# Kernel tuning notes

Measured on AMD Instinct MI355X. Metric: run time of the kernel, lower is better.

Reference implementation:

```python
import jax, jax.numpy as jnp
import numpy as np

N = 50000   # nodes
E = 800000  # edges
D = 128     # input feature dim
HID = 64    # hidden dim
NEG_SLOPE = 0.2


def setup_inputs() -> dict:
    key = jax.random.key(0)
    ks = jax.random.split(key, 12)
    s = 0.1
    x = jax.random.normal(ks[0], (N, D), jnp.float32)
    edge_index = jax.random.randint(ks[1], (2, E), 0, N, dtype=jnp.int64)
    # layer 1: GATConv(128 -> 64, heads=2, concat=False)
    W1 = jax.random.normal(ks[2], (D, 2 * HID), jnp.float32) * s
    a_src1 = jax.random.normal(ks[3], (2, HID), jnp.float32) * s
    a_dst1 = jax.random.normal(ks[4], (2, HID), jnp.float32) * s
    b1 = jnp.zeros((HID,), jnp.float32)
    # layer 2: GATConv(64 -> 64, heads=1, concat=False)
    W2 = jax.random.normal(ks[5], (HID, HID), jnp.float32) * s
    a_src2 = jax.random.normal(ks[6], (1, HID), jnp.float32) * s
    a_dst2 = jax.random.normal(ks[7], (1, HID), jnp.float32) * s
    b2 = jnp.zeros((HID,), jnp.float32)
    # classifier Linear(64 -> 2)
    Wc = jax.random.normal(ks[8], (HID, 2), jnp.float32) * s
    bc = jnp.zeros((2,), jnp.float32)
    return {"x": x, "edge_index": edge_index, "W1": W1, "a_src1": a_src1,
            "a_dst1": a_dst1, "b1": b1, "W2": W2, "a_src2": a_src2,
            "a_dst2": a_dst2, "b2": b2, "Wc": Wc, "bc": bc}


def _gat_layer(x, src, dst, W, a_s, a_d, b, n):
    """PyG GATConv (concat=False -> mean over heads), eval mode."""
    H, C = a_s.shape
    h = (x @ W).reshape(n, H, C)                      # [N,H,C]
    alpha_s = jnp.sum(h * a_s, axis=-1)               # [N,H]
    alpha_d = jnp.sum(h * a_d, axis=-1)               # [N,H]
    e = jax.nn.leaky_relu(alpha_s[src] + alpha_d[dst], NEG_SLOPE)  # [E,H]
    # segment softmax over incoming edges of each target node
    m = jax.ops.segment_max(e, dst, num_segments=n)   # [N,H]
    e = jnp.exp(e - m[dst])
    denom = jax.ops.segment_sum(e, dst, num_segments=n)
    alpha = e / (denom[dst] + 1e-16)                  # [E,H]
    msg = h[src] * alpha[:, :, None]                  # [E,H,C]
    out = jax.ops.segment_sum(msg, dst, num_segments=n)  # [N,H,C]
    return out.mean(axis=1) + b                       # [N,C]


def reference(x, edge_index, W1, a_src1, a_dst1, b1, W2, a_src2, a_dst2, b2, Wc, bc):
    n = x.shape[0]
    loops = jnp.arange(n, dtype=edge_index.dtype)     # PyG add_self_loops=True
    src = jnp.concatenate([edge_index[0], loops])
    dst = jnp.concatenate([edge_index[1], loops])
    h = jax.nn.elu(_gat_layer(x, src, dst, W1, a_src1, a_dst1, b1, n))
    h = jax.nn.elu(_gat_layer(h, src, dst, W2, a_src2, a_dst2, b2, n))
    logits = h @ Wc + bc
    return jax.nn.log_softmax(logits, axis=1)
```

## Files before the change

### kernel.cpp

```cpp
#include <hip/hip_runtime.h>
#include <math.h>

#define NN 50000
#define NE 800000
#define NT (NE + NN)
#define NBUCK 196
#define BE 4096
#define NBLK_B ((NT + BE - 1) / BE)
#define CAP 6144
#define NBLK_G ((NN + 63) / 64)

typedef short bf16x8 __attribute__((ext_vector_type(8)));
typedef float f32x4 __attribute__((ext_vector_type(4)));
union U16x8 { uint4 u; bf16x8 s; };

__device__ __forceinline__ unsigned pk_bf16x2(float x, float y) {
  unsigned ux = __float_as_uint(x); ux = ux + 0x7FFFu + ((ux >> 16) & 1u);
  unsigned uy = __float_as_uint(y); uy = uy + 0x7FFFu + ((uy >> 16) & 1u);
  return (ux >> 16) | (uy & 0xFFFF0000u);
}
__device__ __forceinline__ unsigned short bf16_1(float x) {
  unsigned u = __float_as_uint(x); u = u + 0x7FFFu + ((u >> 16) & 1u);
  return (unsigned short)(u >> 16);
}
__device__ __forceinline__ float blo(unsigned v) { return __uint_as_float(v << 16); }
__device__ __forceinline__ float bhi(unsigned v) { return __uint_as_float(v & 0xFFFF0000u); }

__global__ __launch_bounds__(256) void k_prep(const float* __restrict__ W1, const float* __restrict__ W2,
                                              unsigned short* __restrict__ w1f,
                                              unsigned short* __restrict__ w2f,
                                              int* __restrict__ bcur) {
  int i = blockIdx.x * 256 + threadIdx.x;
  if (i < NBUCK) bcur[i] = i * CAP;
  if (i < 128 * 128) {
    int k = i >> 7, col = i & 127;
    int ct = col >> 4, kt = k >> 5, lane = (((k >> 3) & 3) << 4) | (col & 15), j = k & 7;
    w1f[(((ct << 2) | kt) * 64 + lane) * 8 + j] = bf16_1(W1[i]);
  } else if (i < 128 * 128 + 64 * 64) {
    int e = i - 128 * 128;
    int k = e >> 6, col = e & 63;
    int ct = col >> 4, kt = k >> 5, lane = (((k >> 3) & 3) << 4) | (col & 15), j = k & 7;
    w2f[(((ct << 1) | kt) * 64 + lane) * 8 + j] = bf16_1(W2[e]);
  }
}

__global__ __launch_bounds__(256) void k_gb(
    const int* __restrict__ src, const int* __restrict__ dst,
    int* __restrict__ bcur, unsigned* __restrict__ staging,
    const float* __restrict__ x, const unsigned short* __restrict__ w1f,
    const float* __restrict__ asw_g, const float* __restrict__ adw_g,
    unsigned short* __restrict__ h1b, float* __restrict__ as1, float* __restrict__ ad1) {
  __shared__ int hist[NBUCK];
  __shared__ int base[NBUCK];
  if (blockIdx.x < NBLK_B) {
    const int t = threadIdx.x;
    const int e0 = blockIdx.x * BE;
    if (t < NBUCK) hist[t] = 0;
    __syncthreads();
    for (int j = t; j < BE; j += 256) {
      int i = e0 + j;
      if (i >= NT) break;
      int d = (i < NE) ? dst[i] : (i - NE);
      atomicAdd(&hist[d >> 8], 1);
    }
    __syncthreads();
    if (t < NBUCK) {
      int c = hist[t];
      base[t] = c ? atomicAdd(&bcur[t], c) : 0;
      hist[t] = 0;
    }
    __syncthreads();
    for (int j = t; j < BE; j += 256) {
      int i = e0 + j;
      if (i >= NT) break;
      int s, d;
      if (i < NE) { s = src[i]; d = dst[i]; } else { s = d = i - NE; }
      int b = d >> 8;
      int off = atomicAdd(&hist[b], 1);
      staging[base[b] + off] = ((unsigned)d << 16) | (unsigned)s;
    }
    return;
  }
  const int bid = blockIdx.x - NBLK_B;
  const int t = threadIdx.x;
  const int wid = t >> 6, l = t & 63;
  const int lr = l & 15, lg = l >> 4;
  const int arow = bid * 64 + wid * 16 + lr;
  const bool aok = arow < NN;

  float asw_t[8], adw_t[8];
#pragma unroll
  for (int ct = 0; ct < 8; ++ct) {
    asw_t[ct] = asw_g[ct * 16 + lr];
    adw_t[ct] = adw_g[ct * 16 + lr];
  }

  f32x4 acc[8];
#pragma unroll
  for (int ct = 0; ct < 8; ++ct) acc[ct] = (f32x4){0.f, 0.f, 0.f, 0.f};

#pragma unroll
  for (int kt = 0; kt < 4; ++kt) {
    U16x8 a;
    if (aok) {
      const float* xp = &x[(long long)arow * 128 + kt * 32 + lg * 8];
      float4 f0 = *(const float4*)xp;
      float4 f1 = *(const float4*)(xp + 4);
      a.u.x = pk_bf16x2(f0.x, f0.y); a.u.y = pk_bf16x2(f0.z, f0.w);
      a.u.z = pk_bf16x2(f1.x, f1.y); a.u.w = pk_bf16x2(f1.z, f1.w);
    } else {
      a.u = make_uint4(0, 0, 0, 0);
    }
#pragma unroll
    for (int ct = 0; ct < 8; ++ct) {
      U16x8 b;
      b.u = *(const uint4*)&w1f[(((ct << 2) | kt) * 64 + l) * 8];
      acc[ct] = __builtin_amdgcn_mfma_f32_16x16x32_bf16(a.s, b.s, acc[ct], 0, 0, 0);
    }
  }

  const int gr0 = bid * 64 + wid * 16 + lg * 4;
#pragma unroll
  for (int reg = 0; reg < 4; ++reg) {
    int grow = gr0 + reg;
    bool ok = grow < NN;
    float s0 = 0.f, s1 = 0.f, d0 = 0.f, d1 = 0.f;
#pragma unroll
    for (int ct = 0; ct < 8; ++ct) {
      float v = acc[ct][reg];
      if (ok) h1b[(long long)grow * 128 + ct * 16 + lr] = bf16_1(v);
      if (ct < 4) { s0 += v * asw_t[ct]; d0 += v * adw_t[ct]; }
      else        { s1 += v * asw_t[ct]; d1 += v * adw_t[ct]; }
    }
#pragma unroll
    for (int off = 1; off < 16; off <<= 1) {
      s0 += __shfl_xor(s0, off); d0 += __shfl_xor(d0, off);
      s1 += __shfl_xor(s1, off); d1 += __shfl_xor(d1, off);
    }
    if (ok && lr == 0) {
      as1[grow * 2] = s0; as1[grow * 2 + 1] = s1;
      ad1[grow * 2] = d0; ad1[grow * 2 + 1] = d1;
    }
  }
}

__global__ __launch_bounds__(256) void k_bscan(const int* __restrict__ bcur, int* __restrict__ bbase) {
  __shared__ int wsum[4];
  const int t = threadIdx.x;
  const int l = t & 63, w = t >> 6;
  int v = (t < NBUCK) ? bcur[t] - t * CAP : 0;
  int sc = v;
#pragma unroll
  for (int off = 1; off < 64; off <<= 1) {
    int u = __shfl_up(sc, off);
    if (l >= off) sc += u;
  }
  if (l == 63) wsum[w] = sc;
  __syncthreads();
  int wo = 0;
  for (int i = 0; i < w; ++i) wo += wsum[i];
  int incl = sc + wo;
  if (t < NBUCK) bbase[t] = incl - v;
  if (t == 255) bbase[NBUCK] = incl;
}

__global__ __launch_bounds__(256) void k_scatter2(const unsigned* __restrict__ staging,
                                                  const int* __restrict__ bcur,
                                                  const int* __restrict__ bbase,
                                                  int* __restrict__ rowptr,
                                                  unsigned short* __restrict__ csr16) {
  __shared__ int lcnt[256];
  __shared__ int wsum[4];
  const int b = blockIdx.x;
  const int t = threadIdx.x;
  const int nlo = b << 8;
  lcnt[t] = 0;
  __syncthreads();
  const int s0 = b * CAP;
  const int cnt = bcur[b] - s0;
  for (int k = t; k < cnt; k += 256)
    atomicAdd(&lcnt[(int)(staging[s0 + k] >> 16) - nlo], 1);
  __syncthreads();
  int v = lcnt[t];
  int sc = v;
  const int l = t & 63, w = t >> 6;
#pragma unroll
  for (int off = 1; off < 64; off <<= 1) {
    int u = __shfl_up(sc, off);
    if (l >= off) sc += u;
  }
  if (l == 63) wsum[w] = sc;
  __syncthreads();
  int wo = 0;
  for (int i = 0; i < w; ++i) wo += wsum[i];
  const int base = bbase[b] + sc + wo - v;
  if (nlo + t < NN) rowptr[nlo + t] = base;
  if (b == NBUCK - 1 && t == 0) rowptr[NN] = bbase[NBUCK];
  __syncthreads();
  lcnt[t] = base;
  __syncthreads();
  for (int k = t; k < cnt; k += 256) {
    unsigned e = staging[s0 + k];
    int d = (int)(e >> 16) - nlo;
    int pos = atomicAdd(&lcnt[d], 1);
    csr16[pos] = (unsigned short)(e & 0xFFFFu);
  }
}

__global__ __launch_bounds__(256) void k_gat1(
    const int* __restrict__ rowptr, const unsigned short* __restrict__ csr16,
    const unsigned* __restrict__ h1u, const float2* __restrict__ as1,
    const float2* __restrict__ ad1, const float* __restrict__ b1,
    unsigned* __restrict__ out1b) {
  __shared__ float2 sw[4][2][64];
  const int t = threadIdx.x;
  const int wv = t >> 6;
  const int n = blockIdx.x * 4 + wv;
  if (n >= NN) return;
  const int p = t & 63;
  const int h = p >> 5;
  const int beg = rowptr[n], end = rowptr[n + 1];
  const int deg = end - beg;
  const float2 adn = ad1[n];

  float acc0 = 0.f, acc1 = 0.f;
  float inv;

  if (deg <= 64) {
    int s = 0; float e0 = -1e30f, e1 = -1e30f;
    if (p < deg) {
      s = csr16[beg + p];
      float2 a = as1[s];
      e0 = a.x + adn.x; e0 = fmaxf(e0, 0.2f * e0);
      e1 = a.y + adn.y; e1 = fmaxf(e1, 0.2f * e1);
    }
    float m0 = e0, m1 = e1;
#pragma unroll
    for (int off = 1; off < 64; off <<= 1) {
      m0 = fmaxf(m0, __shfl_xor(m0, off));
      m1 = fmaxf(m1, __shfl_xor(m1, off));
    }
    float w0 = (p < deg) ? __expf(e0 - m0) : 0.f;
    float w1 = (p < deg) ? __expf(e1 - m1) : 0.f;
    float d0 = w0, d1 = w1;
#pragma unroll
    for (int off = 1; off < 64; off <<= 1) {
      d0 += __shfl_xor(d0, off);
      d1 += __shfl_xor(d1, off);
    }
    sw[wv][0][p] = make_float2(__int_as_float(s), w0);
    sw[wv][1][p] = make_float2(__int_as_float(s), w1);
    __builtin_amdgcn_wave_barrier();
    inv = 1.f / ((h ? d1 : d0) + 1e-16f);

    int j = 0;
    for (; j + 8 <= deg; j += 8) {
      float2 a[8]; unsigned v[8];
#pragma unroll
      for (int u = 0; u < 8; ++u) a[u] = sw[wv][h][j + u];
#pragma unroll
      for (int u = 0; u < 8; ++u) v[u] = h1u[(__float_as_int(a[u].x) << 6) + p];
#pragma unroll
      for (int u = 0; u < 8; ++u) {
        acc0 += a[u].y * blo(v[u]);
        acc1 += a[u].y * bhi(v[u]);
      }
    }
    if (j + 4 <= deg) {
      float2 a[4]; unsigned v[4];
#pragma unroll
      for (int u = 0; u < 4; ++u) a[u] = sw[wv][h][j + u];
#pragma unroll
      for (int u = 0; u < 4; ++u) v[u] = h1u[(__float_as_int(a[u].x) << 6) + p];
#pragma unroll
      for (int u = 0; u < 4; ++u) {
        acc0 += a[u].y * blo(v[u]);
        acc1 += a[u].y * bhi(v[u]);
      }
      j += 4;
    }
    for (; j < deg; ++j) {
      float2 a = sw[wv][h][j];
      unsigned v = h1u[(__float_as_int(a.x) << 6) + p];
      acc0 += a.y * blo(v); acc1 += a.y * bhi(v);
    }
  } else {
    float m0 = -1e30f, d0 = 0.f, m1 = -1e30f, d1 = 0.f;
    for (int k = beg + p; k < end; k += 64) {
      float2 a = as1[csr16[k]];
      float e0 = a.x + adn.x; e0 = fmaxf(e0, 0.2f * e0);
      float e1 = a.y + adn.y; e1 = fmaxf(e1, 0.2f * e1);
      if (e0 > m0) { d0 *= __expf(m0 - e0); m0 = e0; }
      d0 += __expf(e0 - m0);
      if (e1 > m1) { d1 *= __expf(m1 - e1); m1 = e1; }
      d1 += __expf(e1 - m1);
    }
#pragma unroll
    for (int off = 1; off < 64; off <<= 1) {
      float mo = __shfl_xor(m0, off), dd = __shfl_xor(d0, off);
      float mn = fmaxf(m0, mo);
      d0 = d0 * __expf(m0 - mn) + dd * __expf(mo - mn);
      m0 = mn;
      mo = __shfl_xor(m1, off); dd = __shfl_xor(d1, off);
      mn = fmaxf(m1, mo);
      d1 = d1 * __expf(m1 - mn) + dd * __expf(mo - mn);
      m1 = mn;
    }
    inv = 1.f / ((h ? d1 : d0) + 1e-16f);
    for (int c0 = beg; c0 < end; c0 += 64) {
      int nc = end - c0; if (nc > 64) nc = 64;
      int s = 0; float w0 = 0.f, w1 = 0.f;
      if (p < nc) {
        s = csr16[c0 + p];
        float2 a = as1[s];
        float e0 = a.x + adn.x; e0 = fmaxf(e0, 0.2f * e0);
        float e1 = a.y + adn.y; e1 = fmaxf(e1, 0.2f * e1);
        w0 = __expf(e0 - m0);
        w1 = __expf(e1 - m1);
      }
      __builtin_amdgcn_wave_barrier();
      sw[wv][0][p] = make_float2(__int_as_float(s), w0);
      sw[wv][1][p] = make_float2(__int_as_float(s), w1);
      __builtin_amdgcn_wave_barrier();
      for (int j = 0; j < nc; ++j) {
        float2 a = sw[wv][h][j];
        unsigned v = h1u[(__float_as_int(a.x) << 6) + p];
        acc0 += a.y * blo(v); acc1 += a.y * bhi(v);
      }
      __builtin_amdgcn_wave_barrier();
    }
  }

  acc0 *= inv; acc1 *= inv;
  acc0 += __shfl_xor(acc0, 32);
  acc1 += __shfl_xor(acc1, 32);
  if (p < 32) {
    float u0 = 0.5f * acc0 + b1[2 * p];
    float u1 = 0.5f * acc1 + b1[2 * p + 1];
    u0 = u0 > 0.f ? u0 : expm1f(u0);
    u1 = u1 > 0.f ? u1 : expm1f(u1);
    out1b[n * 32 + p] = pk_bf16x2(u0, u1);
  }
}

__global__ __launch_bounds__(256) void k_gemm2(
    const unsigned short* __restrict__ in_b, const unsigned short* __restrict__ w2f,
    const float* __restrict__ asw_g, const float* __restrict__ adw_g,
    unsigned short* __restrict__ h2b, float* __restrict__ as2, float* __restrict__ ad2) {
  const int t = threadIdx.x;
  const int wid = t >> 6, l = t & 63;
  const int lr = l & 15, lg = l >> 4;
  const int arow = blockIdx.x * 64 + wid * 16 + lr;
  const bool aok = arow < NN;

  float asw_t[4], adw_t[4];
#pragma unroll
  for (int ct = 0; ct < 4; ++ct) {
    asw_t[ct] = asw_g[ct * 16 + lr];
    adw_t[ct] = adw_g[ct * 16 + lr];
  }

  f32x4 acc[4];
#pragma unroll
  for (int ct = 0; ct < 4; ++ct) acc[ct] = (f32x4){0.f, 0.f, 0.f, 0.f};

#pragma unroll
  for (int kt = 0; kt < 2; ++kt) {
    U16x8 a;
    if (aok) a.u = *(const uint4*)&in_b[(long long)arow * 64 + kt * 32 + lg * 8];
    else a.u = make_uint4(0, 0, 0, 0);
#pragma unroll
    for (int ct = 0; ct < 4; ++ct) {
      U16x8 b;
      b.u = *(const uint4*)&w2f[(((ct << 1) | kt) * 64 + l) * 8];
      acc[ct] = __builtin_amdgcn_mfma_f32_16x16x32_bf16(a.s, b.s, acc[ct], 0, 0, 0);
    }
  }

  const int gr0 = blockIdx.x * 64 + wid * 16 + lg * 4;
#pragma unroll
  for (int reg = 0; reg < 4; ++reg) {
    int grow = gr0 + reg;
    bool ok = grow < NN;
    float s0 = 0.f, d0 = 0.f;
#pragma unroll
    for (int ct = 0; ct < 4; ++ct) {
      float v = acc[ct][reg];
      if (ok) h2b[(long long)grow * 64 + ct * 16 + lr] = bf16_1(v);
      s0 += v * asw_t[ct]; d0 += v * adw_t[ct];
    }
#pragma unroll
    for (int off = 1; off < 16; off <<= 1) {
      s0 += __shfl_xor(s0, off); d0 += __shfl_xor(d0, off);
    }
    if (ok && lr == 0) { as2[grow] = s0; ad2[grow] = d0; }
  }
}

__global__ __launch_bounds__(256) void k_gat2(
    const int* __restrict__ rowptr, const unsigned short* __restrict__ csr16,
    const unsigned* __restrict__ h2u, const float* __restrict__ as2,
    const float* __restrict__ ad2, const float* __restrict__ b2,
    const float* __restrict__ Wc, const float* __restrict__ bc,
    float* __restrict__ out) {
  __shared__ float2 sw[4][64];
  const int t = threadIdx.x;
  const int wv = t >> 6;
  const int n = blockIdx.x * 4 + wv;
  if (n >= NN) return;
  const int p = t & 63;
  const int half = p >> 5;
  const int q = p & 31;
  const int beg = rowptr[n], end = rowptr[n + 1];
  const int deg = end - beg;
  const float adn = ad2[n];

  float acc0 = 0.f, acc1 = 0.f;
  float inv;

  if (deg <= 64) {
    int s = 0; float e = -1e30f;
    if (p < deg) {
      s = csr16[beg + p];
      e = as2[s] + adn;
      e = fmaxf(e, 0.2f * e);
    }
    float m = e;
#pragma unroll
    for (int off = 1; off < 64; off <<= 1) m = fmaxf(m, __shfl_xor(m, off));
    float w = (p < deg) ? __expf(e - m) : 0.f;
    float d = w;
#pragma unroll
    for (int off = 1; off < 64; off <<= 1) d += __shfl_xor(d, off);
    sw[wv][p] = make_float2(__int_as_float(s), w);
    __builtin_amdgcn_wave_barrier();
    inv = 1.f / (d + 1e-16f);

    int niter = (deg + 1) >> 1;
    int i = 0;
    for (; i + 4 <= niter; i += 4) {
      float2 a[4]; unsigned v[4];
#pragma unroll
      for (int u = 0; u < 4; ++u) a[u] = sw[wv][2 * (i + u) + half];
#pragma unroll
      for (int u = 0; u < 4; ++u) v[u] = h2u[(__float_as_int(a[u].x) << 5) + q];
#pragma unroll
      for (int u = 0; u < 4; ++u) {
        acc0 += a[u].y * blo(v[u]);
        acc1 += a[u].y * bhi(v[u]);
      }
    }
    if (i + 2 <= niter) {
      float2 a0 = sw[wv][2 * i + half];
      float2 a1 = sw[wv][2 * (i + 1) + half];
      unsigned v0 = h2u[(__float_as_int(a0.x) << 5) + q];
      unsigned v1 = h2u[(__float_as_int(a1.x) << 5) + q];
      acc0 += a0.y * blo(v0); acc1 += a0.y * bhi(v0);
      acc0 += a1.y * blo(v1); acc1 += a1.y * bhi(v1);
      i += 2;
    }
    if (i < niter) {
      float2 a = sw[wv][2 * i + half];
      unsigned v = h2u[(__float_as_int(a.x) << 5) + q];
      acc0 += a.y * blo(v); acc1 += a.y * bhi(v);
    }
  } else {
    float m = -1e30f, d = 0.f;
    for (int k = beg + p; k < end; k += 64) {
      float e = as2[csr16[k]] + adn;
      e = fmaxf(e, 0.2f * e);
      if (e > m) { d *= __expf(m - e); m = e; }
      d += __expf(e - m);
    }
#pragma unroll
    for (int off = 1; off < 64; off <<= 1) {
      float mo = __shfl_xor(m, off), dd = __shfl_xor(d, off);
      float mn = fmaxf(m, mo);
      d = d * __expf(m - mn) + dd * __expf(mo - mn);
      m = mn;
    }
    inv = 1.f / (d + 1e-16f);
    for (int c0 = beg; c0 < end; c0 += 64) {
      int nc = end - c0; if (nc > 64) nc = 64;
      int s = 0; float w = 0.f;
      if (p < nc) {
        s = csr16[c0 + p];
        float e = as2[s] + adn;
        e = fmaxf(e, 0.2f * e);
        w = __expf(e - m);
      }
      __builtin_amdgcn_wave_barrier();
      sw[wv][p] = make_float2(__int_as_float(s), w);
      __builtin_amdgcn_wave_barrier();
      int niter = (nc + 1) >> 1;
      for (int i = 0; i < niter; ++i) {
        int j = 2 * i + half;
        float2 a = sw[wv][j < nc ? j : 0];
        float wj = (j < nc) ? a.y : 0.f;
        unsigned v = h2u[(__float_as_int(a.x) << 5) + q];
        acc0 += wj * blo(v); acc1 += wj * bhi(v);
      }
      __builtin_amdgcn_wave_barrier();
    }
  }

  acc0 += __shfl_xor(acc0, 32);
  acc1 += __shfl_xor(acc1, 32);
  float v0 = acc0 * inv + b2[2 * q];
  float v1 = acc1 * inv + b2[2 * q + 1];
  v0 = v0 > 0.f ? v0 : expm1f(v0);
  v1 = v1 > 0.f ? v1 : expm1f(v1);
  float l0 = v0 * Wc[4 * q] + v1 * Wc[4 * q + 2];
  float l1 = v0 * Wc[4 * q + 1] + v1 * Wc[4 * q + 3];
#pragma unroll
  for (int off = 1; off < 32; off <<= 1) {
    l0 += __shfl_xor(l0, off);
    l1 += __shfl_xor(l1, off);
  }
  if (p == 0) {
    l0 += bc[0]; l1 += bc[1];
    float mx = fmaxf(l0, l1);
    float lse = mx + logf(expf(l0 - mx) + expf(l1 - mx));
    out[n * 2] = l0 - lse;
    out[n * 2 + 1] = l1 - lse;
  }
}

extern "C" void kernel_launch(void* const* d_in, const int* in_sizes, int n_in,
                              void* d_out, int out_size, void* d_ws, size_t ws_size,
                              hipStream_t stream) {
  const float* x    = (const float*)d_in[0];
  const int*   ei   = (const int*)d_in[1];
  const float* W1   = (const float*)d_in[2];
  const float* as1w = (const float*)d_in[3];
  const float* ad1w = (const float*)d_in[4];
  const float* b1   = (const float*)d_in[5];
  const float* W2   = (const float*)d_in[6];
  const float* as2w = (const float*)d_in[7];
  const float* ad2w = (const float*)d_in[8];
  const float* b2   = (const float*)d_in[9];
  const float* Wc   = (const float*)d_in[10];
  const float* bc   = (const float*)d_in[11];
  float* out = (float*)d_out;

  const int* src = ei;
  const int* dst = ei + NE;

  char* p = (char*)d_ws;
  unsigned short* h1b = (unsigned short*)p; p += sizeof(unsigned short) * (long long)NN * 128;
  unsigned short* out1b = (unsigned short*)p; p += sizeof(unsigned short) * (long long)NN * 64;
  unsigned short* h2b = (unsigned short*)p; p += sizeof(unsigned short) * (long long)NN * 64;
  float* as1  = (float*)p; p += sizeof(float) * NN * 2;
  float* ad1  = (float*)p; p += sizeof(float) * NN * 2;
  float* as2  = (float*)p; p += sizeof(float) * NN;
  float* ad2  = (float*)p; p += sizeof(float) * NN;
  int* rowptr  = (int*)p; p += sizeof(int) * (NN + 64);
  int* bcur    = (int*)p; p += sizeof(int) * ((NBUCK + 63) & ~63);
  int* bbase   = (int*)p; p += sizeof(int) * ((NBUCK + 64) & ~63);
  unsigned* staging = (unsigned*)p; p += sizeof(unsigned) * (long long)NBUCK * CAP;
  unsigned short* csr16 = (unsigned short*)p; p += sizeof(unsigned short) * (long long)NT;
  unsigned short* w1f = (unsigned short*)p; p += sizeof(unsigned short) * 128 * 128;
  unsigned short* w2f = (unsigned short*)p; p += sizeof(unsigned short) * 64 * 64;

  k_prep<<<(128 * 128 + 64 * 64 + 255) / 256, 256, 0, stream>>>(W1, W2, w1f, w2f, bcur);
  k_gb<<<NBLK_B + NBLK_G, 256, 0, stream>>>(src, dst, bcur, staging,
                                            x, w1f, as1w, ad1w, h1b, as1, ad1);
  k_bscan<<<1, 256, 0, stream>>>(bcur, bbase);
  k_scatter2<<<NBUCK, 256, 0, stream>>>(staging, bcur, bbase, rowptr, csr16);

  k_gat1<<<(NN + 3) / 4, 256, 0, stream>>>(rowptr, csr16, (const unsigned*)h1b,
                                           (const float2*)as1, (const float2*)ad1, b1,
                                           (unsigned*)out1b);

  k_gemm2<<<(NN + 63) / 64, 256, 0, stream>>>(out1b, w2f, as2w, ad2w, h2b, as2, ad2);
  k_gat2<<<(NN + 3) / 4, 256, 0, stream>>>(rowptr, csr16, (const unsigned*)h2b,
                                           as2, ad2, b2, Wc, bc, out);
}
```

Before: 116.1 us.

## Fuse bucket scan into scatter and process two nodes per wave in gat1

The single-block bucket prefix scan kernel is removed. Every scatter block now recomputes the scan over all bucket counts redundantly, which eliminates one launch and one serial dependency. In layer-1 aggregation each wave now handles two destination nodes, one per half-wave. Each lane gathers 8 bytes (uint2) of the neighbour feature row instead of 4, which doubles the gather width per lane and halves the number of blocks. The cost is a narrower 32-lane reduction per node and some redundant scan work in every scatter block.

```diff
diff --git a/kernel.cpp b/kernel.cpp
--- a/kernel.cpp
+++ b/kernel.cpp
@@ -144,58 +144,57 @@
   }
 }
 
-__global__ __launch_bounds__(256) void k_bscan(const int* __restrict__ bcur, int* __restrict__ bbase) {
-  __shared__ int wsum[4];
-  const int t = threadIdx.x;
-  const int l = t & 63, w = t >> 6;
-  int v = (t < NBUCK) ? bcur[t] - t * CAP : 0;
-  int sc = v;
-#pragma unroll
-  for (int off = 1; off < 64; off <<= 1) {
-    int u = __shfl_up(sc, off);
-    if (l >= off) sc += u;
-  }
-  if (l == 63) wsum[w] = sc;
-  __syncthreads();
-  int wo = 0;
-  for (int i = 0; i < w; ++i) wo += wsum[i];
-  int incl = sc + wo;
-  if (t < NBUCK) bbase[t] = incl - v;
-  if (t == 255) bbase[NBUCK] = incl;
-}
-
 __global__ __launch_bounds__(256) void k_scatter2(const unsigned* __restrict__ staging,
                                                   const int* __restrict__ bcur,
-                                                  const int* __restrict__ bbase,
                                                   int* __restrict__ rowptr,
                                                   unsigned short* __restrict__ csr16) {
   __shared__ int lcnt[256];
   __shared__ int wsum[4];
+  __shared__ int sOff, sTot;
   const int b = blockIdx.x;
   const int t = threadIdx.x;
   const int nlo = b << 8;
+  const int l = t & 63, w = t >> 6;
+
+  int bc = (t < NBUCK) ? bcur[t] - t * CAP : 0;
+  int sc = bc;
+#pragma unroll
+  for (int off = 1; off < 64; off <<= 1) {
+    int u = __shfl_up(sc, off);
+    if (l >= off) sc += u;
+  }
+  if (l == 63) wsum[w] = sc;
+  __syncthreads();
+  {
+    int wo = 0;
+    for (int i = 0; i < w; ++i) wo += wsum[i];
+    int incl = sc + wo;
+    if (t == b) sOff = incl - bc;
+    if (t == 255) sTot = incl;
+  }
   lcnt[t] = 0;
   __syncthreads();
+
   const int s0 = b * CAP;
   const int cnt = bcur[b] - s0;
   for (int k = t; k < cnt; k += 256)
     atomicAdd(&lcnt[(int)(staging[s0 + k] >> 16) - nlo], 1);
   __syncthreads();
   int v = lcnt[t];
-  int sc = v;
-  const int l = t & 63, w = t >> 6;
+  int sc2 = v;
 #pragma unroll
   for (int off = 1; off < 64; off <<= 1) {
-    int u = __shfl_up(sc, off);
-    if (l >= off) sc += u;
-  }
-  if (l == 63) wsum[w] = sc;
+    int u = __shfl_up(sc2, off);
+    if (l >= off) sc2 += u;
+  }
+  __syncthreads();
+  if (l == 63) wsum[w] = sc2;
   __syncthreads();
   int wo = 0;
   for (int i = 0; i < w; ++i) wo += wsum[i];
-  const int base = bbase[b] + sc + wo - v;
+  const int base = sOff + sc2 + wo - v;
   if (nlo + t < NN) rowptr[nlo + t] = base;
-  if (b == NBUCK - 1 && t == 0) rowptr[NN] = bbase[NBUCK];
+  if (b == NBUCK - 1 && t == 0) rowptr[NN] = sTot;
   __syncthreads();
   lcnt[t] = base;
   __syncthreads();
@@ -209,84 +208,99 @@
 
 __global__ __launch_bounds__(256) void k_gat1(
     const int* __restrict__ rowptr, const unsigned short* __restrict__ csr16,
-    const unsigned* __restrict__ h1u, const float2* __restrict__ as1,
+    const uint2* __restrict__ h1x2, const float2* __restrict__ as1,
     const float2* __restrict__ ad1, const float* __restrict__ b1,
-    unsigned* __restrict__ out1b) {
-  __shared__ float2 sw[4][2][64];
+    uint2* __restrict__ out1x2) {
+  __shared__ float4 sw[4][2][64];
   const int t = threadIdx.x;
   const int wv = t >> 6;
-  const int n = blockIdx.x * 4 + wv;
+  const int p = t & 63;
+  const int hw = p >> 5;
+  const int l = p & 31;
+  const int n = blockIdx.x * 8 + wv * 2 + hw;
   if (n >= NN) return;
-  const int p = t & 63;
-  const int h = p >> 5;
   const int beg = rowptr[n], end = rowptr[n + 1];
   const int deg = end - beg;
   const float2 adn = ad1[n];
-
-  float acc0 = 0.f, acc1 = 0.f;
+  const int hd = l >> 4;
+
+  float a0 = 0.f, a1 = 0.f, a2 = 0.f, a3 = 0.f;
   float inv;
 
   if (deg <= 64) {
-    int s = 0; float e0 = -1e30f, e1 = -1e30f;
-    if (p < deg) {
-      s = csr16[beg + p];
-      float2 a = as1[s];
-      e0 = a.x + adn.x; e0 = fmaxf(e0, 0.2f * e0);
-      e1 = a.y + adn.y; e1 = fmaxf(e1, 0.2f * e1);
-    }
-    float m0 = e0, m1 = e1;
-#pragma unroll
-    for (int off = 1; off < 64; off <<= 1) {
+    int sA = 0, sB = 0;
+    float e0A = -1e30f, e1A = -1e30f, e0B = -1e30f, e1B = -1e30f;
+    if (l < deg) {
+      sA = csr16[beg + l];
+      float2 a = as1[sA];
+      e0A = a.x + adn.x; e0A = fmaxf(e0A, 0.2f * e0A);
+      e1A = a.y + adn.y; e1A = fmaxf(e1A, 0.2f * e1A);
+    }
+    if (l + 32 < deg) {
+      sB = csr16[beg + l + 32];
+      float2 a = as1[sB];
+      e0B = a.x + adn.x; e0B = fmaxf(e0B, 0.2f * e0B);
+      e1B = a.y + adn.y; e1B = fmaxf(e1B, 0.2f * e1B);
+    }
+    float m0 = fmaxf(e0A, e0B), m1 = fmaxf(e1A, e1B);
+#pragma unroll
+    for (int off = 1; off < 32; off <<= 1) {
       m0 = fmaxf(m0, __shfl_xor(m0, off));
       m1 = fmaxf(m1, __shfl_xor(m1, off));
     }
-    float w0 = (p < deg) ? __expf(e0 - m0) : 0.f;
-    float w1 = (p < deg) ? __expf(e1 - m1) : 0.f;
-    float d0 = w0, d1 = w1;
-#pragma unroll
-    for (int off = 1; off < 64; off <<= 1) {
+    float w0A = (l < deg) ? __expf(e0A - m0) : 0.f;
+    float w1A = (l < deg) ? __expf(e1A - m1) : 0.f;
+    float w0B = (l + 32 < deg) ? __expf(e0B - m0) : 0.f;
+    float w1B = (l + 32 < deg) ? __expf(e1B - m1) : 0.f;
+    float d0 = w0A + w0B, d1 = w1A + w1B;
+#pragma unroll
+    for (int off = 1; off < 32; off <<= 1) {
       d0 += __shfl_xor(d0, off);
       d1 += __shfl_xor(d1, off);
     }
-    sw[wv][0][p] = make_float2(__int_as_float(s), w0);
-    sw[wv][1][p] = make_float2(__int_as_float(s), w1);
+    sw[wv][hw][l]      = make_float4(__int_as_float(sA), w0A, w1A, 0.f);
+    sw[wv][hw][l + 32] = make_float4(__int_as_float(sB), w0B, w1B, 0.f);
     __builtin_amdgcn_wave_barrier();
-    inv = 1.f / ((h ? d1 : d0) + 1e-16f);
+    inv = 1.f / ((hd ? d1 : d0) + 1e-16f);
 
     int j = 0;
     for (; j + 8 <= deg; j += 8) {
-      float2 a[8]; unsigned v[8];
-#pragma unroll
-      for (int u = 0; u < 8; ++u) a[u] = sw[wv][h][j + u];
-#pragma unroll
-      for (int u = 0; u < 8; ++u) v[u] = h1u[(__float_as_int(a[u].x) << 6) + p];
+      float4 a[8]; uint2 v[8];
+#pragma unroll
+      for (int u = 0; u < 8; ++u) a[u] = sw[wv][hw][j + u];
+#pragma unroll
+      for (int u = 0; u < 8; ++u) v[u] = h1x2[(__float_as_int(a[u].x) << 5) + l];
 #pragma unroll
       for (int u = 0; u < 8; ++u) {
-        acc0 += a[u].y * blo(v[u]);
-        acc1 += a[u].y * bhi(v[u]);
+        float wgt = hd ? a[u].z : a[u].y;
+        a0 += wgt * blo(v[u].x); a1 += wgt * bhi(v[u].x);
+        a2 += wgt * blo(v[u].y); a3 += wgt * bhi(v[u].y);
       }
     }
     if (j + 4 <= deg) {
-      float2 a[4]; unsigned v[4];
-#pragma unroll
-      for (int u = 0; u < 4; ++u) a[u] = sw[wv][h][j + u];
-#pragma unroll
-      for (int u = 0; u < 4; ++u) v[u] = h1u[(__float_as_int(a[u].x) << 6) + p];
+      float4 a[4]; uint2 v[4];
+#pragma unroll
+      for (int u = 0; u < 4; ++u) a[u] = sw[wv][hw][j + u];
+#pragma unroll
+      for (int u = 0; u < 4; ++u) v[u] = h1x2[(__float_as_int(a[u].x) << 5) + l];
 #pragma unroll
       for (int u = 0; u < 4; ++u) {
-        acc0 += a[u].y * blo(v[u]);
-        acc1 += a[u].y * bhi(v[u]);
+        float wgt = hd ? a[u].z : a[u].y;
+        a0 += wgt * blo(v[u].x); a1 += wgt * bhi(v[u].x);
+        a2 += wgt * blo(v[u].y); a3 += wgt * bhi(v[u].y);
       }
       j += 4;
     }
     for (; j < deg; ++j) {
-      float2 a = sw[wv][h][j];
-      unsigned v = h1u[(__float_as_int(a.x) << 6) + p];
-      acc0 += a.y * blo(v); acc1 += a.y * bhi(v);
+      float4 a = sw[wv][hw][j];
+      uint2 v = h1x2[(__float_as_int(a.x) << 5) + l];
+      float wgt = hd ? a.z : a.y;
+      a0 += wgt * blo(v.x); a1 += wgt * bhi(v.x);
+      a2 += wgt * blo(v.y); a3 += wgt * bhi(v.y);
     }
   } else {
     float m0 = -1e30f, d0 = 0.f, m1 = -1e30f, d1 = 0.f;
-    for (int k = beg + p; k < end; k += 64) {
+    for (int k = beg + l; k < end; k += 32) {
       float2 a = as1[csr16[k]];
       float e0 = a.x + adn.x; e0 = fmaxf(e0, 0.2f * e0);
       float e1 = a.y + adn.y; e1 = fmaxf(e1, 0.2f * e1);
@@ -296,7 +310,7 @@
       d1 += __expf(e1 - m1);
     }
 #pragma unroll
-    for (int off = 1; off < 64; off <<= 1) {
+    for (int off = 1; off < 32; off <<= 1) {
       float mo = __shfl_xor(m0, off), dd = __shfl_xor(d0, off);
       float mn = fmaxf(m0, mo);
       d0 = d0 * __expf(m0 - mn) + dd * __expf(mo - mn);
@@ -306,40 +320,52 @@
       d1 = d1 * __expf(m1 - mn) + dd * __expf(mo - mn);
       m1 = mn;
     }
-    inv = 1.f / ((h ? d1 : d0) + 1e-16f);
+    inv = 1.f / ((hd ? d1 : d0) + 1e-16f);
     for (int c0 = beg; c0 < end; c0 += 64) {
       int nc = end - c0; if (nc > 64) nc = 64;
-      int s = 0; float w0 = 0.f, w1 = 0.f;
-      if (p < nc) {
-        s = csr16[c0 + p];
-        float2 a = as1[s];
+      int sA = 0, sB = 0; float w0A = 0.f, w1A = 0.f, w0B = 0.f, w1B = 0.f;
+      if (l < nc) {
+        sA = csr16[c0 + l];
+        float2 a = as1[sA];
         float e0 = a.x + adn.x; e0 = fmaxf(e0, 0.2f * e0);
         float e1 = a.y + adn.y; e1 = fmaxf(e1, 0.2f * e1);
-        w0 = __expf(e0 - m0);
-        w1 = __expf(e1 - m1);
+        w0A = __expf(e0 - m0); w1A = __expf(e1 - m1);
+      }
+      if (l + 32 < nc) {
+        sB = csr16[c0 + l + 32];
+        float2 a = as1[sB];
+        float e0 = a.x + adn.x; e0 = fmaxf(e0, 0.2f * e0);
+        float e1 = a.y + adn.y; e1 = fmaxf(e1, 0.2f * e1);
+        w0B = __expf(e0 - m0); w1B = __expf(e1 - m1);
       }
       __builtin_amdgcn_wave_barrier();
-      sw[wv][0][p] = make_float2(__int_as_float(s), w0);
-      sw[wv][1][p] = make_float2(__int_as_float(s), w1);
+      sw[wv][hw][l]      = make_float4(__int_as_float(sA), w0A, w1A, 0.f);
+      sw[wv][hw][l + 32] = make_float4(__int_as_float(sB), w0B, w1B, 0.f);
       __builtin_amdgcn_wave_barrier();
       for (int j = 0; j < nc; ++j) {
-        float2 a = sw[wv][h][j];
-        unsigned v = h1u[(__float_as_int(a.x) << 6) + p];
-        acc0 += a.y * blo(v); acc1 += a.y * bhi(v);
+        float4 a = sw[wv][hw][j];
+        uint2 v = h1x2[(__float_as_int(a.x) << 5) + l];
+        float wgt = hd ? a.z : a.y;
+        a0 += wgt * blo(v.x); a1 += wgt * bhi(v.x);
+        a2 += wgt * blo(v.y); a3 += wgt * bhi(v.y);
       }
       __builtin_amdgcn_wave_barrier();
     }
   }
 
-  acc0 *= inv; acc1 *= inv;
-  acc0 += __shfl_xor(acc0, 32);
-  acc1 += __shfl_xor(acc1, 32);
-  if (p < 32) {
-    float u0 = 0.5f * acc0 + b1[2 * p];
-    float u1 = 0.5f * acc1 + b1[2 * p + 1];
+  a0 *= inv; a1 *= inv; a2 *= inv; a3 *= inv;
+  float c0 = __shfl_xor(a0, 16), c1 = __shfl_xor(a1, 16),
+        c2 = __shfl_xor(a2, 16), c3 = __shfl_xor(a3, 16);
+  if (l < 16) {
+    float u0 = 0.5f * (a0 + c0) + b1[4 * l + 0];
+    float u1 = 0.5f * (a1 + c1) + b1[4 * l + 1];
+    float u2 = 0.5f * (a2 + c2) + b1[4 * l + 2];
+    float u3 = 0.5f * (a3 + c3) + b1[4 * l + 3];
     u0 = u0 > 0.f ? u0 : expm1f(u0);
     u1 = u1 > 0.f ? u1 : expm1f(u1);
-    out1b[n * 32 + p] = pk_bf16x2(u0, u1);
+    u2 = u2 > 0.f ? u2 : expm1f(u2);
+    u3 = u3 > 0.f ? u3 : expm1f(u3);
+    out1x2[n * 16 + l] = make_uint2(pk_bf16x2(u0, u1), pk_bf16x2(u2, u3));
   }
 }
 
@@ -556,7 +582,6 @@
   float* ad2  = (float*)p; p += sizeof(float) * NN;
   int* rowptr  = (int*)p; p += sizeof(int) * (NN + 64);
   int* bcur    = (int*)p; p += sizeof(int) * ((NBUCK + 63) & ~63);
-  int* bbase   = (int*)p; p += sizeof(int) * ((NBUCK + 64) & ~63);
   unsigned* staging = (unsigned*)p; p += sizeof(unsigned) * (long long)NBUCK * CAP;
   unsigned short* csr16 = (unsigned short*)p; p += sizeof(unsigned short) * (long long)NT;
   unsigned short* w1f = (unsigned short*)p; p += sizeof(unsigned short) * 128 * 128;
@@ -565,12 +590,11 @@
   k_prep<<<(128 * 128 + 64 * 64 + 255) / 256, 256, 0, stream>>>(W1, W2, w1f, w2f, bcur);
   k_gb<<<NBLK_B + NBLK_G, 256, 0, stream>>>(src, dst, bcur, staging,
                                             x, w1f, as1w, ad1w, h1b, as1, ad1);
-  k_bscan<<<1, 256, 0, stream>>>(bcur, bbase);
-  k_scatter2<<<NBUCK, 256, 0, stream>>>(staging, bcur, bbase, rowptr, csr16);
-
-  k_gat1<<<(NN + 3) / 4, 256, 0, stream>>>(rowptr, csr16, (const unsigned*)h1b,
+  k_scatter2<<<NBUCK, 256, 0, stream>>>(staging, bcur, rowptr, csr16);
+
+  k_gat1<<<(NN + 7) / 8, 256, 0, stream>>>(rowptr, csr16, (const uint2*)h1b,
                                            (const float2*)as1, (const float2*)ad1, b1,
-                                           (unsigned*)out1b);
+                                           (uint2*)out1b);
 
   k_gemm2<<<(NN + 63) / 64, 256, 0, stream>>>(out1b, w2f, as2w, ad2w, h2b, as2, ad2);
   k_gat2<<<(NN + 3) / 4, 256, 0, stream>>>(rowptr, csr16, (const unsigned*)h2b,
```

Result: no change. 116.3 us (+0.2%).
